# Optimization experiments

Measured on AMD Instinct MI355X. Metric: run time of the kernel, lower is better.

## Reference

```python
import jax, jax.numpy as jnp
import numpy as np

N_NODES = 100000
N_EDGES = 1600000
IN_FEATS = 128
HID = 32
N_REL = 5
N_BASES = 2
N_PAIRS = 4096


def setup_inputs() -> dict:
    key = jax.random.key(0)
    ks = jax.random.split(key, 24)
    d = {}
    d['x'] = jax.random.normal(ks[0], (N_NODES, IN_FEATS), dtype=jnp.float32)
    d['edge_mask'] = jnp.ones((N_EDGES,), dtype=jnp.float32)
    d['etype'] = jax.random.randint(ks[1], (N_EDGES,), 0, N_REL, dtype=jnp.int32)
    d['src'] = jax.random.randint(ks[2], (N_EDGES,), 0, N_NODES, dtype=jnp.int32)
    d['dst'] = jax.random.randint(ks[3], (N_EDGES,), 0, N_NODES, dtype=jnp.int32)
    d['users_idx'] = jax.random.randint(ks[4], (N_PAIRS,), 0, N_NODES, dtype=jnp.int32)
    d['items_idx'] = jax.random.randint(ks[5], (N_PAIRS,), 0, N_NODES, dtype=jnp.int32)
    # RelGraphConv params (basis decomposition): layer1 in->32, layers 2,3 32->32
    def s(k, din):
        return 1.0 / np.sqrt(din)
    d['V1'] = jax.random.normal(ks[6], (N_BASES, IN_FEATS, HID), dtype=jnp.float32) * s(0, IN_FEATS)
    d['comp1'] = jax.random.normal(ks[7], (N_REL, N_BASES), dtype=jnp.float32)
    d['loop1'] = jax.random.normal(ks[8], (IN_FEATS, HID), dtype=jnp.float32) * s(0, IN_FEATS)
    d['b1'] = jnp.zeros((HID,), dtype=jnp.float32)
    d['V2'] = jax.random.normal(ks[9], (N_BASES, HID, HID), dtype=jnp.float32) * s(0, HID)
    d['comp2'] = jax.random.normal(ks[10], (N_REL, N_BASES), dtype=jnp.float32)
    d['loop2'] = jax.random.normal(ks[11], (HID, HID), dtype=jnp.float32) * s(0, HID)
    d['b2'] = jnp.zeros((HID,), dtype=jnp.float32)
    d['V3'] = jax.random.normal(ks[12], (N_BASES, HID, HID), dtype=jnp.float32) * s(0, HID)
    d['comp3'] = jax.random.normal(ks[13], (N_REL, N_BASES), dtype=jnp.float32)
    d['loop3'] = jax.random.normal(ks[14], (HID, HID), dtype=jnp.float32) * s(0, HID)
    d['b3'] = jnp.zeros((HID,), dtype=jnp.float32)
    # MLP head: lin1 (2*sum(latent_dim[1:]) = 192 -> 128), lin2 (128 -> 1)
    d['w1'] = jax.random.normal(ks[15], (2 * 3 * HID, 128), dtype=jnp.float32) * (1.0 / np.sqrt(2 * 3 * HID))
    d['bw1'] = jnp.zeros((128,), dtype=jnp.float32)
    d['w2'] = jax.random.normal(ks[16], (128, 1), dtype=jnp.float32) * (1.0 / np.sqrt(128))
    d['bw2'] = jnp.zeros((1,), dtype=jnp.float32)
    return d


def _rgcn_layer(x, V, comp, loopw, bias, etype, src, dst, norm):
    # basis-decomposed relational conv: W_r = sum_b comp[r,b] * V[b]
    xb = jnp.einsum('nd,bdo->nbo', x, V)                       # [N,B,O]
    msg = jnp.einsum('eb,ebo->eo', comp[etype], xb[src])       # [E,O]
    msg = msg * norm[:, None]                                  # edge_mask norm
    agg = jax.ops.segment_sum(msg, dst, num_segments=x.shape[0])
    return jnp.tanh(agg + x @ loopw + bias)


def reference(x, edge_mask, etype, src, dst, users_idx, items_idx,
              V1, comp1, loop1, b1, V2, comp2, loop2, b2, V3, comp3, loop3, b3,
              w1, bw1, w2, bw2):
    h1 = _rgcn_layer(x, V1, comp1, loop1, b1, etype, src, dst, edge_mask)
    h2 = _rgcn_layer(h1, V2, comp2, loop2, b2, etype, src, dst, edge_mask)
    h3 = _rgcn_layer(h2, V3, comp3, loop3, b3, etype, src, dst, edge_mask)
    concat_states = jnp.concatenate([h1, h2, h3], axis=1)      # [N, 96]
    feats = jnp.concatenate([concat_states[users_idx], concat_states[items_idx]], axis=1)  # [P,192]
    hidden = jax.nn.relu(feats @ w1 + bw1)
    out = hidden @ w2 + bw2
    return out[:, 0]  # multiply_by = 1
```

## Files before the change

### kernel.cpp

```cpp
#include <hip/hip_runtime.h>
#include <stdint.h>

#define N_NODES  100000
#define N_EDGES  1600000
#define IN_FEATS 128
#define HID      32
#define N_REL    5
#define N_BASES  2
#define N_PAIRS  4096

#define NB        196
#define BCAP      16384
#define EPB       2048
#define SC_BLOCKS 782
#define TL1_BLOCKS 1250

typedef __attribute__((ext_vector_type(8))) short short8;
typedef __attribute__((ext_vector_type(4))) float f32x4;

__device__ inline unsigned int pack_bf16(float a, float b) {
    unsigned int ua = __float_as_uint(a), ub = __float_as_uint(b);
    ua = (ua + 0x7fffu + ((ua >> 16) & 1u)) >> 16;
    ub = (ub + 0x7fffu + ((ub >> 16) & 1u)) >> 16;
    return ua | (ub << 16);
}

__device__ inline unsigned short bf16_1(float a) {
    unsigned int u = __float_as_uint(a);
    u = (u + 0x7fffu + ((u >> 16) & 1u)) >> 16;
    return (unsigned short)u;
}

__device__ inline void split_bf16_2(float a, float b, unsigned int& hi, unsigned int& lo) {
    unsigned int ha = bf16_1(a), hb = bf16_1(b);
    hi = ha | (hb << 16);
    float fa = __uint_as_float(ha << 16), fb = __uint_as_float(hb << 16);
    lo = pack_bf16(a - fa, b - fb);
}


__global__ __launch_bounds__(256) void k_wprep(
    const float* __restrict__ V1, const float* __restrict__ comp1, const float* __restrict__ loop1,
    const float* __restrict__ V2, const float* __restrict__ loop2,
    const float* __restrict__ V3, const float* __restrict__ loop3,
    unsigned short* __restrict__ Wbf1, unsigned short* __restrict__ Wcat2,
    unsigned short* __restrict__ Wcat3, int* __restrict__ gcur) {
    int b = blockIdx.x;
    int t = threadIdx.x;
    if (b == 0 && t < NB) gcur[t] = 0;
    if (b < 96) {
        int idx = b * 256 + t;
        if (idx >= 192 * IN_FEATS) return;
        int j = idx / IN_FEATS, k = idx % IN_FEATS;
        float v;
        if (j < 160) {
            int r = j >> 5, o = j & 31;
            v = comp1[r * 2 + 0] * V1[(size_t)(0 * IN_FEATS + k) * 32 + o]
              + comp1[r * 2 + 1] * V1[(size_t)(1 * IN_FEATS + k) * 32 + o];
        } else {
            v = loop1[k * 32 + (j - 160)];
        }
        Wbf1[idx] = bf16_1(v);
        return;
    }
    const float *V, *loopw;
    unsigned short* Wc;
    int idx;
    if (b < 116) { V = V2; loopw = loop2; Wc = Wcat2; idx = (b - 96) * 256 + t; }
    else         { V = V3; loopw = loop3; Wc = Wcat3; idx = (b - 116) * 256 + t; }
    if (idx >= 32 * 160) return;
    int col = idx / 160, k = idx % 160;
    int seg = k >> 5, inner = k & 31;
    float v;
    if (seg < 2)      v = V[inner * 32 + col];
    else if (seg < 4) v = V[(32 + inner) * 32 + col];
    else              v = loopw[inner * 32 + col];
    Wc[idx] = bf16_1(v);
}


#define SMEM_BYTES 23856

__global__ __launch_bounds__(256) void k_fused1(
    const int* __restrict__ src, const int* __restrict__ dst,
    const int* __restrict__ etype, const float* __restrict__ mask,
    int* __restrict__ gcur, int2* __restrict__ ebuf,
    const float* __restrict__ xin,
    const unsigned short* __restrict__ Wbf, const float* __restrict__ bias,
    unsigned short* __restrict__ xs16, float* __restrict__ aggout) {
    __shared__ __attribute__((aligned(16))) char smem[SMEM_BYTES];
    int b = blockIdx.x;
    int t = threadIdx.x;
    if (b < SC_BLOCKS) {
        int2*  srec    = (int2*)smem;
        short* sb      = (short*)(smem + 16384);
        int*   lh      = (int*)(smem + 20480);
        int*   lex     = (int*)(smem + 21264);
        int*   gbase   = (int*)(smem + 22048);
        int*   scanbuf = (int*)(smem + 22832);
        int e0 = b * EPB;
        if (t < NB) lh[t] = 0;
        __syncthreads();
        int2 rec[8];
        int  bk[8];
#pragma unroll
        for (int i = 0; i < 8; i++) {
            int e = e0 + t + i * 256;
            if (e < N_EDGES) {
                int d = dst[e];
                bk[i] = d >> 9;
                rec[i].x = ((d & 511) << 23) | (src[e] << 4) | etype[e];
                rec[i].y = __float_as_int(mask[e]);
                atomicAdd(&lh[bk[i]], 1);
            } else bk[i] = -1;
        }
        __syncthreads();
        int cnt = (t < NB) ? lh[t] : 0;
        scanbuf[t] = cnt;
        __syncthreads();
        for (int off = 1; off < 256; off <<= 1) {
            int v = (t >= off) ? scanbuf[t - off] : 0;
            __syncthreads();
            scanbuf[t] += v;
            __syncthreads();
        }
        if (t < NB) {
            lex[t] = scanbuf[t] - cnt;
            gbase[t] = t * BCAP + (cnt ? atomicAdd(&gcur[t], cnt) : 0);
            lh[t] = 0;
        }
        __syncthreads();
#pragma unroll
        for (int i = 0; i < 8; i++) {
            if (bk[i] >= 0) {
                int p = lex[bk[i]] + atomicAdd(&lh[bk[i]], 1);
                srec[p] = rec[i];
                sb[p] = (short)bk[i];
            }
        }
        __syncthreads();
        int total = scanbuf[NB - 1];
        for (int idx = t; idx < total; idx += 256) {
            int bb = sb[idx];
            ebuf[gbase[bb] + (idx - lex[bb])] = srec[idx];
        }
        return;
    }
    unsigned short* As = (unsigned short*)smem;
    unsigned short* tb = (unsigned short*)(smem + 4352);
    int bb = b - SC_BLOCKS;
    int wv = t >> 6, lane = t & 63;
    int q = lane >> 4, n16 = lane & 15;
    short8 bfr[3][4];
#pragma unroll
    for (int i = 0; i < 3; i++) {
        int tt = wv * 3 + i;
#pragma unroll
        for (int ks = 0; ks < 4; ks++)
            bfr[i][ks] = *(const short8*)(Wbf + (tt * 16 + n16) * 128 + ks * 32 + q * 8);
    }
    float bv0 = bias[n16], bv1 = bias[16 + n16];
    int node_l = t >> 4;
    int seg    = t & 15;
    int g0 = bb * 5;
    float4 p0, p1;
    {
        const float* xr = xin + ((size_t)(g0 * 16 + node_l)) * 128 + seg * 8;
        p0 = *(const float4*)xr;
        p1 = *(const float4*)(xr + 4);
    }
    for (int gi = 0; gi < 5; gi++) {
        int g = g0 + gi;
        int n0 = g * 16;
        __syncthreads();
        {
            uint4 v;
            v.x = pack_bf16(p0.x, p0.y);
            v.y = pack_bf16(p0.z, p0.w);
            v.z = pack_bf16(p1.x, p1.y);
            v.w = pack_bf16(p1.z, p1.w);
            *(uint4*)(As + node_l * 136 + seg * 8) = v;
        }
        __syncthreads();
        if (gi + 1 < 5) {
            const float* xr = xin + ((size_t)((g + 1) * 16 + node_l)) * 128 + seg * 8;
            p0 = *(const float4*)xr;
            p1 = *(const float4*)(xr + 4);
        }
        short8 afr[4];
#pragma unroll
        for (int ks = 0; ks < 4; ks++)
            afr[ks] = *(const short8*)(As + n16 * 136 + ks * 32 + q * 8);
        f32x4 d[3];
        f32x4 z = {0.f, 0.f, 0.f, 0.f};
#pragma unroll
        for (int i = 0; i < 3; i++) d[i] = z;
#pragma unroll
        for (int i = 0; i < 3; i++)
#pragma unroll
            for (int ks = 0; ks < 4; ks++)
                d[i] = __builtin_amdgcn_mfma_f32_16x16x32_bf16(afr[ks], bfr[i][ks], d[i], 0, 0, 0);
#pragma unroll
        for (int i = 0; i < 3; i++) {
            int tt = wv * 3 + i;
            if (tt < 10) {
#pragma unroll
                for (int r = 0; r < 4; r++)
                    tb[(q * 4 + r) * 168 + tt * 16 + n16] = bf16_1(d[i][r]);
            } else {
                float bv = (tt == 10) ? bv0 : bv1;
                int o = (tt - 10) * 16 + n16;
#pragma unroll
                for (int r = 0; r < 4; r++) {
                    int node = n0 + q * 4 + r;
                    aggout[(size_t)node * 32 + o] = d[i][r] + bv;
                }
            }
        }
        __syncthreads();
        for (int c = t; c < 320; c += 256) {
            int node_i = c / 20, part = c % 20;
            short8 vv = *(const short8*)(tb + node_i * 168 + part * 8);
            *(short8*)(xs16 + (size_t)(n0 + node_i) * 160 + part * 8) = vv;
        }
    }
}


__global__ __launch_bounds__(512) void k_bsort2(
    const int* __restrict__ gcur, const int2* __restrict__ ebuf,
    int2* __restrict__ esort, int* __restrict__ offsets) {
    __shared__ int hist[512];
    __shared__ int incl[512];
    __shared__ int cur[512];
    __shared__ int bs[256];
    __shared__ int sBase, sCnt;
    int blk = blockIdx.x, b = blk >> 1, h = blk & 1, t = threadIdx.x;
    if (t < 256) bs[t] = (t < NB) ? gcur[t] : 0;
    __syncthreads();
    for (int off = 1; off < 256; off <<= 1) {
        int v = 0;
        if (t < 256 && t >= off) v = bs[t - off];
        __syncthreads();
        if (t < 256) bs[t] += v;
        __syncthreads();
    }
    if (t == 0) { sCnt = gcur[b]; sBase = bs[b] - gcur[b]; }
    hist[t] = 0;
    __syncthreads();
    int cnt = sCnt, gbase = sBase;
    const int2* slab = ebuf + (size_t)b * BCAP;
    for (int e = t; e < cnt; e += 512) {
        int dl = ((unsigned)slab[e].x) >> 23;
        atomicAdd(&hist[dl], 1);
    }
    __syncthreads();
    incl[t] = hist[t];
    __syncthreads();
    for (int off = 1; off < 512; off <<= 1) {
        int v = 0;
        if (t >= off) v = incl[t - off];
        __syncthreads();
        incl[t] += v;
        __syncthreads();
    }
    int ex = incl[t] - hist[t];
    cur[t] = ex;
    if ((t >> 8) == h) {
        int n = (b << 9) + t;
        if (n <= N_NODES) offsets[n] = gbase + ex;
    }
    if (b == NB - 1 && h == 1 && t == 0) offsets[N_NODES] = N_EDGES;
    __syncthreads();
    for (int e = t; e < cnt; e += 512) {
        int2 pk = slab[e];
        int dl = ((unsigned)pk.x) >> 23;
        if ((dl >> 8) == h) {
            int pos = gbase + atomicAdd(&cur[dl], 1);
            int2 rec;
            rec.x = pk.x & 0x7fffff;
            rec.y = pk.y;
            esort[pos] = rec;
        }
    }
}


__global__ __launch_bounds__(256) void k_agg1(
    const int* __restrict__ offsets, const int2* __restrict__ esort,
    const unsigned int* __restrict__ xrel16, const float* __restrict__ agg,
    float* __restrict__ concat, unsigned int* __restrict__ hrel_out) {
    int v = blockIdx.x * 32 + (threadIdx.x >> 3);
    int o = threadIdx.x & 7;
    int s0 = offsets[v], s1 = offsets[v + 1];
    float4 a0 = *(const float4*)(agg + (size_t)v * 32 + o * 4);
    float acc0 = a0.x, acc1 = a0.y, acc2 = a0.z, acc3 = a0.w;
    int last = s1 - 1;
    for (int e = s0; e < s1; e += 16) {
        int addr[16];
        float m[16];
#pragma unroll
        for (int i = 0; i < 16; i++) {
            int ei = e + i;
            int ec = (ei <= last) ? ei : last;
            int2 pk = esort[ec];
            int low = pk.x;
            addr[i] = (low >> 4) * 80 + (low & 15) * 16;
            m[i] = (ei <= last) ? __int_as_float(pk.y) : 0.f;
        }
        uint2 xw[16];
#pragma unroll
        for (int i = 0; i < 16; i++)
            xw[i] = *(const uint2*)(xrel16 + (unsigned)addr[i] + o * 2);
#pragma unroll
        for (int i = 0; i < 16; i++) {
            float f0 = __uint_as_float(xw[i].x << 16);
            float f1 = __uint_as_float(xw[i].x & 0xffff0000u);
            float f2 = __uint_as_float(xw[i].y << 16);
            float f3 = __uint_as_float(xw[i].y & 0xffff0000u);
            acc0 = fmaf(m[i], f0, acc0);
            acc1 = fmaf(m[i], f1, acc1);
            acc2 = fmaf(m[i], f2, acc2);
            acc3 = fmaf(m[i], f3, acc3);
        }
    }
    float4 r;
    r.x = tanhf(acc0); r.y = tanhf(acc1); r.z = tanhf(acc2); r.w = tanhf(acc3);
    *(float4*)(concat + (size_t)v * 96 + o * 4) = r;
    hrel_out[v * 16 + o * 2]     = pack_bf16(r.x, r.y);
    hrel_out[v * 16 + o * 2 + 1] = pack_bf16(r.z, r.w);
}


__global__ __launch_bounds__(256) void k_agg23(
    const int* __restrict__ offsets, const int2* __restrict__ esort,
    const unsigned int* __restrict__ hrel_in, const float* __restrict__ comp,
    const unsigned short* __restrict__ Wcat, const float* __restrict__ bias,
    float* __restrict__ concat, int hoff, unsigned int* __restrict__ hrel_out) {
    __shared__ unsigned int hbf[32][84];
    __shared__ float2 cLds[5];
    int t = threadIdx.x;
    if (t < 5) cLds[t] = ((const float2*)comp)[t];
    int nl = t >> 3;
    int v = blockIdx.x * 32 + nl;
    int o = t & 7;
    int s0 = offsets[v], s1 = offsets[v + 1];
    __syncthreads();
    float y00 = 0.f, y01 = 0.f, y02 = 0.f, y03 = 0.f;
    float y10 = 0.f, y11 = 0.f, y12 = 0.f, y13 = 0.f;
    int last = s1 - 1;
    for (int e = s0; e < s1; e += 16) {
        int addr[16];
        float c0[16], c1[16];
#pragma unroll
        for (int i = 0; i < 16; i++) {
            int ei = e + i;
            int ec = (ei <= last) ? ei : last;
            int2 pk = esort[ec];
            int low = pk.x;
            addr[i] = low & 0x7ffff0;
            float2 cc = cLds[low & 15];
            float m = (ei <= last) ? __int_as_float(pk.y) : 0.f;
            c0[i] = m * cc.x;
            c1[i] = m * cc.y;
        }
        uint2 xw[16];
#pragma unroll
        for (int i = 0; i < 16; i++)
            xw[i] = *(const uint2*)(hrel_in + (unsigned)addr[i] + o * 2);
#pragma unroll
        for (int i = 0; i < 16; i++) {
            float f0 = __uint_as_float(xw[i].x << 16);
            float f1 = __uint_as_float(xw[i].x & 0xffff0000u);
            float f2 = __uint_as_float(xw[i].y << 16);
            float f3 = __uint_as_float(xw[i].y & 0xffff0000u);
            y00 = fmaf(c0[i], f0, y00); y10 = fmaf(c1[i], f0, y10);
            y01 = fmaf(c0[i], f1, y01); y11 = fmaf(c1[i], f1, y11);
            y02 = fmaf(c0[i], f2, y02); y12 = fmaf(c1[i], f2, y12);
            y03 = fmaf(c0[i], f3, y03); y13 = fmaf(c1[i], f3, y13);
        }
    }
    unsigned int hi, lo;
    split_bf16_2(y00, y01, hi, lo);
    hbf[nl][o * 2]          = hi;  hbf[nl][16 + o * 2]     = lo;
    split_bf16_2(y02, y03, hi, lo);
    hbf[nl][o * 2 + 1]      = hi;  hbf[nl][16 + o * 2 + 1] = lo;
    split_bf16_2(y10, y11, hi, lo);
    hbf[nl][32 + o * 2]     = hi;  hbf[nl][48 + o * 2]     = lo;
    split_bf16_2(y12, y13, hi, lo);
    hbf[nl][32 + o * 2 + 1] = hi;  hbf[nl][48 + o * 2 + 1] = lo;
    *(uint2*)&hbf[nl][64 + o * 2] = *(const uint2*)(hrel_in + v * 16 + o * 2);
    __syncthreads();
    int wv = t >> 6, lane = t & 63;
    int q = lane >> 4, n16 = lane & 15;
    int gg = wv & 1;
    int tt = wv >> 1;
    f32x4 d = {0.f, 0.f, 0.f, 0.f};
#pragma unroll
    for (int ks = 0; ks < 5; ks++) {
        short8 afr = *(const short8*)&hbf[gg * 16 + n16][ks * 16 + q * 4];
        short8 bfr = *(const short8*)(Wcat + (tt * 16 + n16) * 160 + ks * 32 + q * 8);
        d = __builtin_amdgcn_mfma_f32_16x16x32_bf16(afr, bfr, d, 0, 0, 0);
    }
    float bv = bias[tt * 16 + n16];
    int n0 = blockIdx.x * 32 + gg * 16;
#pragma unroll
    for (int r = 0; r < 4; r++) {
        int node = n0 + q * 4 + r;
        float h = tanhf(d[r] + bv);
        concat[(size_t)node * 96 + hoff + tt * 16 + n16] = h;
        if (hrel_out)
            ((unsigned short*)hrel_out)[node * 32 + tt * 16 + n16] = bf16_1(h);
    }
}


__global__ void k_mlp(const float* __restrict__ concat, const int* __restrict__ uidx,
                      const int* __restrict__ iidx,
                      const float* __restrict__ w1, const float* __restrict__ bw1,
                      const float* __restrict__ w2, const float* __restrict__ bw2,
                      float* __restrict__ out) {
    __shared__ float feats[192];
    __shared__ float red[2];
    int p = blockIdx.x;
    int t = threadIdx.x;
    int u = uidx[p], it = iidx[p];
    for (int k = t; k < 192; k += 128)
        feats[k] = (k < 96) ? concat[(size_t)u * 96 + k] : concat[(size_t)it * 96 + (k - 96)];
    __syncthreads();
    float acc = bw1[t];
    for (int k = 0; k < 192; k++) acc += feats[k] * w1[k * 128 + t];
    float h = fmaxf(acc, 0.f);
    float part = h * w2[t];
    for (int off = 32; off > 0; off >>= 1) part += __shfl_down(part, off, 64);
    if ((t & 63) == 0) red[t >> 6] = part;
    __syncthreads();
    if (t == 0) out[p] = red[0] + red[1] + bw2[0];
}


extern "C" void kernel_launch(void* const* d_in, const int* in_sizes, int n_in,
                              void* d_out, int out_size, void* d_ws, size_t ws_size,
                              hipStream_t stream) {
    const float* x         = (const float*)d_in[0];
    const float* edge_mask = (const float*)d_in[1];
    const int*   etype     = (const int*)d_in[2];
    const int*   src       = (const int*)d_in[3];
    const int*   dst       = (const int*)d_in[4];
    const int*   users_idx = (const int*)d_in[5];
    const int*   items_idx = (const int*)d_in[6];
    const float* V1        = (const float*)d_in[7];
    const float* comp1     = (const float*)d_in[8];
    const float* loop1     = (const float*)d_in[9];
    const float* b1        = (const float*)d_in[10];
    const float* V2        = (const float*)d_in[11];
    const float* comp2     = (const float*)d_in[12];
    const float* loop2     = (const float*)d_in[13];
    const float* b2        = (const float*)d_in[14];
    const float* V3        = (const float*)d_in[15];
    const float* comp3     = (const float*)d_in[16];
    const float* loop3     = (const float*)d_in[17];
    const float* b3        = (const float*)d_in[18];
    const float* w1        = (const float*)d_in[19];
    const float* bw1       = (const float*)d_in[20];
    const float* w2        = (const float*)d_in[21];
    const float* bw2       = (const float*)d_in[22];
    float* out = (float*)d_out;

    uintptr_t w = (uintptr_t)d_ws;
    auto al = [&](size_t bytes) { uintptr_t p = (w + 255) & ~(uintptr_t)255; w = p + bytes; return p; };
    int*   gcur    = (int*)al(sizeof(int) * NB);
    int*   offsets = (int*)al(sizeof(int) * (N_NODES + 1));
    int2*  ebuf    = (int2*)al(sizeof(int2) * (size_t)NB * BCAP);
    unsigned int* xs16  = (unsigned int*)al(sizeof(unsigned int) * (size_t)N_NODES * 80);
    unsigned int* hrel1 = (unsigned int*)al(sizeof(unsigned int) * (size_t)N_NODES * 16);
    unsigned int* hrel2 = (unsigned int*)al(sizeof(unsigned int) * (size_t)N_NODES * 16);
    int2*  esort   = (int2*)al(sizeof(int2) * N_EDGES);
    unsigned short* Wbf1  = (unsigned short*)al(sizeof(unsigned short) * 192 * IN_FEATS);
    unsigned short* Wcat2 = (unsigned short*)al(sizeof(unsigned short) * 32 * 160);
    unsigned short* Wcat3 = (unsigned short*)al(sizeof(unsigned short) * 32 * 160);
    float* aggA    = (float*)al(sizeof(float) * (size_t)N_NODES * 32);
    float* concat  = (float*)al(sizeof(float) * (size_t)N_NODES * 96);

    k_wprep<<<136, 256, 0, stream>>>(V1, comp1, loop1, V2, loop2, V3, loop3,
                                     Wbf1, Wcat2, Wcat3, gcur);
    k_fused1<<<SC_BLOCKS + TL1_BLOCKS, 256, 0, stream>>>(
        src, dst, etype, edge_mask, gcur, ebuf,
        x, Wbf1, b1, (unsigned short*)xs16, aggA);
    k_bsort2<<<2 * NB, 512, 0, stream>>>(gcur, ebuf, esort, offsets);

    const int agrid = N_NODES / 32;

    k_agg1<<<agrid, 256, 0, stream>>>(offsets, esort, xs16, aggA, concat, hrel1);
    k_agg23<<<agrid, 256, 0, stream>>>(offsets, esort, hrel1, comp2, Wcat2, b2,
                                       concat, 32, hrel2);
    k_agg23<<<agrid, 256, 0, stream>>>(offsets, esort, hrel2, comp3, Wcat3, b3,
                                       concat, 64, (unsigned int*)nullptr);

    k_mlp<<<N_PAIRS, 128, 0, stream>>>(concat, users_idx, items_idx, w1, bw1, w2, bw2, out);
}
```

Measured before the change: 318.8 us.

## Regroup kernels: fuse scatter with weight prep, bucket sort with layer-1 transform

```diff
diff --git a/kernel.cpp b/kernel.cpp
--- a/kernel.cpp
+++ b/kernel.cpp
@@ -13,7 +13,9 @@
 #define BCAP      16384
 #define EPB       2048
 #define SC_BLOCKS 782
-#define TL1_BLOCKS 1250
+#define WP_BLOCKS 136
+#define NBSORT    392
+#define TD_BLOCKS 625
 
 typedef __attribute__((ext_vector_type(8))) short short8;
 typedef __attribute__((ext_vector_type(4))) float f32x4;
@@ -39,55 +41,17 @@
 }
 
 
-__global__ __launch_bounds__(256) void k_wprep(
+#define SMEM_BYTES 23856
+
+__global__ __launch_bounds__(256) void k_scatter_wprep(
+    const int* __restrict__ src, const int* __restrict__ dst,
+    const int* __restrict__ etype, const float* __restrict__ mask,
+    int* __restrict__ gcur, int2* __restrict__ ebuf,
     const float* __restrict__ V1, const float* __restrict__ comp1, const float* __restrict__ loop1,
     const float* __restrict__ V2, const float* __restrict__ loop2,
     const float* __restrict__ V3, const float* __restrict__ loop3,
     unsigned short* __restrict__ Wbf1, unsigned short* __restrict__ Wcat2,
-    unsigned short* __restrict__ Wcat3, int* __restrict__ gcur) {
-    int b = blockIdx.x;
-    int t = threadIdx.x;
-    if (b == 0 && t < NB) gcur[t] = 0;
-    if (b < 96) {
-        int idx = b * 256 + t;
-        if (idx >= 192 * IN_FEATS) return;
-        int j = idx / IN_FEATS, k = idx % IN_FEATS;
-        float v;
-        if (j < 160) {
-            int r = j >> 5, o = j & 31;
-            v = comp1[r * 2 + 0] * V1[(size_t)(0 * IN_FEATS + k) * 32 + o]
-              + comp1[r * 2 + 1] * V1[(size_t)(1 * IN_FEATS + k) * 32 + o];
-        } else {
-            v = loop1[k * 32 + (j - 160)];
-        }
-        Wbf1[idx] = bf16_1(v);
-        return;
-    }
-    const float *V, *loopw;
-    unsigned short* Wc;
-    int idx;
-    if (b < 116) { V = V2; loopw = loop2; Wc = Wcat2; idx = (b - 96) * 256 + t; }
-    else         { V = V3; loopw = loop3; Wc = Wcat3; idx = (b - 116) * 256 + t; }
-    if (idx >= 32 * 160) return;
-    int col = idx / 160, k = idx % 160;
-    int seg = k >> 5, inner = k & 31;
-    float v;
-    if (seg < 2)      v = V[inner * 32 + col];
-    else if (seg < 4) v = V[(32 + inner) * 32 + col];
-    else              v = loopw[inner * 32 + col];
-    Wc[idx] = bf16_1(v);
-}
-
-
-#define SMEM_BYTES 23856
-
-__global__ __launch_bounds__(256) void k_fused1(
-    const int* __restrict__ src, const int* __restrict__ dst,
-    const int* __restrict__ etype, const float* __restrict__ mask,
-    int* __restrict__ gcur, int2* __restrict__ ebuf,
-    const float* __restrict__ xin,
-    const unsigned short* __restrict__ Wbf, const float* __restrict__ bias,
-    unsigned short* __restrict__ xs16, float* __restrict__ aggout) {
+    unsigned short* __restrict__ Wcat3) {
     __shared__ __attribute__((aligned(16))) char smem[SMEM_BYTES];
     int b = blockIdx.x;
     int t = threadIdx.x;
@@ -146,10 +110,112 @@
         }
         return;
     }
-    unsigned short* As = (unsigned short*)smem;
-    unsigned short* tb = (unsigned short*)(smem + 4352);
-    int bb = b - SC_BLOCKS;
-    int wv = t >> 6, lane = t & 63;
+    int wb = b - SC_BLOCKS;
+    if (wb < 96) {
+        int idx = wb * 256 + t;
+        if (idx >= 192 * IN_FEATS) return;
+        int j = idx / IN_FEATS, k = idx % IN_FEATS;
+        float v;
+        if (j < 160) {
+            int r = j >> 5, o = j & 31;
+            v = comp1[r * 2 + 0] * V1[(size_t)(0 * IN_FEATS + k) * 32 + o]
+              + comp1[r * 2 + 1] * V1[(size_t)(1 * IN_FEATS + k) * 32 + o];
+        } else {
+            v = loop1[k * 32 + (j - 160)];
+        }
+        Wbf1[idx] = bf16_1(v);
+        return;
+    }
+    const float *V, *loopw;
+    unsigned short* Wc;
+    int idx;
+    if (wb < 116) { V = V2; loopw = loop2; Wc = Wcat2; idx = (wb - 96) * 256 + t; }
+    else          { V = V3; loopw = loop3; Wc = Wcat3; idx = (wb - 116) * 256 + t; }
+    if (idx >= 32 * 160) return;
+    int col = idx / 160, k = idx % 160;
+    int seg = k >> 5, inner = k & 31;
+    float v;
+    if (seg < 2)      v = V[inner * 32 + col];
+    else if (seg < 4) v = V[(32 + inner) * 32 + col];
+    else              v = loopw[inner * 32 + col];
+    Wc[idx] = bf16_1(v);
+}
+
+
+#define SMEM2_BYTES 19456
+
+__global__ __launch_bounds__(512) void k_bsort_tl1(
+    const int* __restrict__ gcur, const int2* __restrict__ ebuf,
+    int2* __restrict__ esort, int* __restrict__ offsets,
+    const float* __restrict__ xin,
+    const unsigned short* __restrict__ Wbf, const float* __restrict__ bias,
+    unsigned short* __restrict__ xs16, float* __restrict__ aggout) {
+    __shared__ __attribute__((aligned(16))) char smem2[SMEM2_BYTES];
+    int b = blockIdx.x;
+    int t = threadIdx.x;
+    if (b < NBSORT) {
+        int* hist = (int*)smem2;
+        int* incl = (int*)(smem2 + 2048);
+        int* cur  = (int*)(smem2 + 4096);
+        int* bs   = (int*)(smem2 + 6144);
+        int* sBC  = (int*)(smem2 + 7168);
+        int bb = b >> 1, h = b & 1;
+        if (t < 256) bs[t] = (t < NB) ? gcur[t] : 0;
+        __syncthreads();
+        for (int off = 1; off < 256; off <<= 1) {
+            int v = 0;
+            if (t < 256 && t >= off) v = bs[t - off];
+            __syncthreads();
+            if (t < 256) bs[t] += v;
+            __syncthreads();
+        }
+        if (t == 0) { sBC[1] = gcur[bb]; sBC[0] = bs[bb] - gcur[bb]; }
+        hist[t] = 0;
+        __syncthreads();
+        int cnt = sBC[1], gbase = sBC[0];
+        const int2* slab = ebuf + (size_t)bb * BCAP;
+        for (int e = t; e < cnt; e += 512) {
+            int dl = ((unsigned)slab[e].x) >> 23;
+            atomicAdd(&hist[dl], 1);
+        }
+        __syncthreads();
+        incl[t] = hist[t];
+        __syncthreads();
+        for (int off = 1; off < 512; off <<= 1) {
+            int v = 0;
+            if (t >= off) v = incl[t - off];
+            __syncthreads();
+            incl[t] += v;
+            __syncthreads();
+        }
+        int ex = incl[t] - hist[t];
+        cur[t] = ex;
+        if ((t >> 8) == h) {
+            int n = (bb << 9) + t;
+            if (n <= N_NODES) offsets[n] = gbase + ex;
+        }
+        if (bb == NB - 1 && h == 1 && t == 0) offsets[N_NODES] = N_EDGES;
+        __syncthreads();
+        for (int e = t; e < cnt; e += 512) {
+            int2 pk = slab[e];
+            int dl = ((unsigned)pk.x) >> 23;
+            if ((dl >> 8) == h) {
+                int pos = gbase + atomicAdd(&cur[dl], 1);
+                int2 rec;
+                rec.x = pk.x & 0x7fffff;
+                rec.y = pk.y;
+                esort[pos] = rec;
+            }
+        }
+        return;
+    }
+    int half = t >> 8;
+    int tl   = t & 255;
+    char* basep = smem2 + half * 9728;
+    unsigned short* As = (unsigned short*)basep;
+    unsigned short* tb = (unsigned short*)(basep + 4352);
+    int bb = (b - NBSORT) * 2 + half;
+    int wv = tl >> 6, lane = tl & 63;
     int q = lane >> 4, n16 = lane & 15;
     short8 bfr[3][4];
 #pragma unroll
@@ -160,8 +226,8 @@
             bfr[i][ks] = *(const short8*)(Wbf + (tt * 16 + n16) * 128 + ks * 32 + q * 8);
     }
     float bv0 = bias[n16], bv1 = bias[16 + n16];
-    int node_l = t >> 4;
-    int seg    = t & 15;
+    int node_l = tl >> 4;
+    int seg    = tl & 15;
     int g0 = bb * 5;
     float4 p0, p1;
     {
@@ -218,69 +284,10 @@
             }
         }
         __syncthreads();
-        for (int c = t; c < 320; c += 256) {
+        for (int c = tl; c < 320; c += 256) {
             int node_i = c / 20, part = c % 20;
             short8 vv = *(const short8*)(tb + node_i * 168 + part * 8);
             *(short8*)(xs16 + (size_t)(n0 + node_i) * 160 + part * 8) = vv;
-        }
-    }
-}
-
-
-__global__ __launch_bounds__(512) void k_bsort2(
-    const int* __restrict__ gcur, const int2* __restrict__ ebuf,
-    int2* __restrict__ esort, int* __restrict__ offsets) {
-    __shared__ int hist[512];
-    __shared__ int incl[512];
-    __shared__ int cur[512];
-    __shared__ int bs[256];
-    __shared__ int sBase, sCnt;
-    int blk = blockIdx.x, b = blk >> 1, h = blk & 1, t = threadIdx.x;
-    if (t < 256) bs[t] = (t < NB) ? gcur[t] : 0;
-    __syncthreads();
-    for (int off = 1; off < 256; off <<= 1) {
-        int v = 0;
-        if (t < 256 && t >= off) v = bs[t - off];
-        __syncthreads();
-        if (t < 256) bs[t] += v;
-        __syncthreads();
-    }
-    if (t == 0) { sCnt = gcur[b]; sBase = bs[b] - gcur[b]; }
-    hist[t] = 0;
-    __syncthreads();
-    int cnt = sCnt, gbase = sBase;
-    const int2* slab = ebuf + (size_t)b * BCAP;
-    for (int e = t; e < cnt; e += 512) {
-        int dl = ((unsigned)slab[e].x) >> 23;
-        atomicAdd(&hist[dl], 1);
-    }
-    __syncthreads();
-    incl[t] = hist[t];
-    __syncthreads();
-    for (int off = 1; off < 512; off <<= 1) {
-        int v = 0;
-        if (t >= off) v = incl[t - off];
-        __syncthreads();
-        incl[t] += v;
-        __syncthreads();
-    }
-    int ex = incl[t] - hist[t];
-    cur[t] = ex;
-    if ((t >> 8) == h) {
-        int n = (b << 9) + t;
-        if (n <= N_NODES) offsets[n] = gbase + ex;
-    }
-    if (b == NB - 1 && h == 1 && t == 0) offsets[N_NODES] = N_EDGES;
-    __syncthreads();
-    for (int e = t; e < cnt; e += 512) {
-        int2 pk = slab[e];
-        int dl = ((unsigned)pk.x) >> 23;
-        if ((dl >> 8) == h) {
-            int pos = gbase + atomicAdd(&cur[dl], 1);
-            int2 rec;
-            rec.x = pk.x & 0x7fffff;
-            rec.y = pk.y;
-            esort[pos] = rec;
         }
     }
 }
@@ -482,12 +489,14 @@
     float* aggA    = (float*)al(sizeof(float) * (size_t)N_NODES * 32);
     float* concat  = (float*)al(sizeof(float) * (size_t)N_NODES * 96);
 
-    k_wprep<<<136, 256, 0, stream>>>(V1, comp1, loop1, V2, loop2, V3, loop3,
-                                     Wbf1, Wcat2, Wcat3, gcur);
-    k_fused1<<<SC_BLOCKS + TL1_BLOCKS, 256, 0, stream>>>(
+    hipMemsetAsync(gcur, 0, sizeof(int) * NB, stream);
+
+    k_scatter_wprep<<<SC_BLOCKS + WP_BLOCKS, 256, 0, stream>>>(
         src, dst, etype, edge_mask, gcur, ebuf,
+        V1, comp1, loop1, V2, loop2, V3, loop3, Wbf1, Wcat2, Wcat3);
+    k_bsort_tl1<<<NBSORT + TD_BLOCKS, 512, 0, stream>>>(
+        gcur, ebuf, esort, offsets,
         x, Wbf1, b1, (unsigned short*)xs16, aggA);
-    k_bsort2<<<2 * NB, 512, 0, stream>>>(gcur, ebuf, esort, offsets);
 
     const int agrid = N_NODES / 32;
 
```

Measured after the change: 318.8 us. Within noise of the previous version (+0.0%).
